# Kernel optimization log

Measured on AMD Instinct MI355X. Metric: run time of the kernel, lower is better.

Reference implementation:

```python
import jax, jax.numpy as jnp
import numpy as np

N = 50000
E = 1600000
D_IN, H1, H2, N_CLS = 512, 128, 64, 10


def _add_self_loops(edge_index, n, edge_attr=None):
    loops = jnp.arange(n, dtype=edge_index.dtype)
    ei = jnp.concatenate([edge_index, jnp.stack([loops, loops])], axis=1)
    if edge_attr is None:
        return ei, None
    # PyG fill_value='mean' for self-loop edge attributes
    loop_attr = jnp.broadcast_to(jnp.mean(edge_attr, axis=0, keepdims=True), (n, edge_attr.shape[1]))
    return ei, jnp.concatenate([edge_attr, loop_attr], axis=0)


def _gat_conv(x, src, dst, n, W, a_src, a_dst, bias, edge_attr=None, We=None, a_edge=None):
    # single-head GATConv
    h = x @ W                                   # (N, out)
    alpha = (h * a_src).sum(-1)[src] + (h * a_dst).sum(-1)[dst]  # (E,)
    if edge_attr is not None:
        alpha = alpha + ((edge_attr @ We) * a_edge).sum(-1)
    alpha = jax.nn.leaky_relu(alpha, 0.2)
    # segment softmax over incoming edges of each dst node
    m = jax.ops.segment_max(alpha, dst, num_segments=n)
    e = jnp.exp(alpha - m[dst])
    s = jax.ops.segment_sum(e, dst, num_segments=n)
    coef = e / (s[dst] + 1e-16)
    out = jax.ops.segment_sum(h[src] * coef[:, None], dst, num_segments=n)
    return out + bias


def _prelu(x, a):
    return jnp.where(x >= 0, x, a * x)


def setup_inputs() -> dict:
    key = jax.random.key(0)
    ks = jax.random.split(key, 24)
    g = lambda k, shape, scale: (jax.random.normal(k, shape, dtype=jnp.float32) * scale)
    inp = {
        "x": jax.random.normal(ks[0], (N, D_IN), dtype=jnp.float32),
        "edge_index": jax.random.randint(ks[1], (2, E), 0, N, dtype=jnp.int32),
        "ppmi_edge_index": jax.random.randint(ks[2], (2, E), 0, N, dtype=jnp.int32),
        "ppmi_edge_attr": jax.random.uniform(ks[3], (E, 1), dtype=jnp.float32),
        # adjacency-branch GAT params
        "W1": g(ks[4], (D_IN, H1), (1.0 / D_IN) ** 0.5),
        "att_src1": g(ks[5], (H1,), 0.1), "att_dst1": g(ks[6], (H1,), 0.1),
        "b1": jnp.zeros((H1,), jnp.float32),
        "W2": g(ks[7], (H1, H2), (1.0 / H1) ** 0.5),
        "att_src2": g(ks[8], (H2,), 0.1), "att_dst2": g(ks[9], (H2,), 0.1),
        "b2": jnp.zeros((H2,), jnp.float32),
        "prelu_a": jnp.float32(0.25),
        # ppmi-branch GAT params (with edge_dim=1)
        "pW1": g(ks[10], (D_IN, H1), (1.0 / D_IN) ** 0.5),
        "patt_src1": g(ks[11], (H1,), 0.1), "patt_dst1": g(ks[12], (H1,), 0.1),
        "pWe1": g(ks[13], (1, H1), 1.0), "patt_e1": g(ks[14], (H1,), 0.1),
        "pb1": jnp.zeros((H1,), jnp.float32),
        "pW2": g(ks[15], (H1, H2), (1.0 / H1) ** 0.5),
        "patt_src2": g(ks[16], (H2,), 0.1), "patt_dst2": g(ks[17], (H2,), 0.1),
        "pWe2": g(ks[18], (1, H2), 1.0), "patt_e2": g(ks[19], (H2,), 0.1),
        "pb2": jnp.zeros((H2,), jnp.float32),
        "pprelu_a": jnp.float32(0.25),
        # fusion attention (Linear(64,1))
        "attn_w": g(ks[20], (H2,), (1.0 / H2) ** 0.5),
        "attn_b": jnp.zeros((), jnp.float32),
        # classifier
        "clf_w": g(ks[21], (H2, N_CLS), (2.0 / H2) ** 0.5),
        "clf_b": jnp.full((N_CLS,), 0.1, jnp.float32),
    }
    return inp


def reference(x, edge_index, ppmi_edge_index, ppmi_edge_attr,
              W1, att_src1, att_dst1, b1, W2, att_src2, att_dst2, b2, prelu_a,
              pW1, patt_src1, patt_dst1, pWe1, patt_e1, pb1,
              pW2, patt_src2, patt_dst2, pWe2, patt_e2, pb2, pprelu_a,
              attn_w, attn_b, clf_w, clf_b):
    n = x.shape[0]
    # adjacency branch (GCN class, GATConv without edge_attr)
    ei, _ = _add_self_loops(edge_index, n)
    src, dst = ei[0], ei[1]
    f1 = _prelu(_gat_conv(x, src, dst, n, W1, att_src1, att_dst1, b1), prelu_a)
    l_out = _prelu(_gat_conv(f1, src, dst, n, W2, att_src2, att_dst2, b2), prelu_a)
    # ppmi branch (GATConv with scalar edge attributes)
    pei, pea = _add_self_loops(ppmi_edge_index, n, ppmi_edge_attr)
    psrc, pdst = pei[0], pei[1]
    g1 = _prelu(_gat_conv(x, psrc, pdst, n, pW1, patt_src1, patt_dst1, pb1, pea, pWe1, patt_e1), pprelu_a)
    g_out = _prelu(_gat_conv(g1, psrc, pdst, n, pW2, patt_src2, patt_dst2, pb2, pea, pWe2, patt_e2), pprelu_a)
    # attn_mode == 1: softmax fusion over stacked branch embeddings
    stacked = jnp.stack([l_out, g_out], axis=1)             # (N, 2, H2)
    scores = stacked @ attn_w + attn_b                      # (N, 2)
    w = jax.nn.softmax(scores, axis=1)[..., None]           # (N, 2, 1)
    emb = jnp.sum(stacked * w, axis=1)                      # (N, H2)
    pred = emb @ clf_w + clf_b                              # (N, n_classes)
    return (emb, pred)
```

## Files before the change

kernel.cpp:

```cpp
#include <hip/hip_runtime.h>
#include <hip/hip_fp16.h>


static constexpr int D_IN = 512;
static constexpr int H1c  = 128;
static constexpr int H2c  = 64;
static constexpr int NCLS = 10;

#define DEV __device__ __forceinline__

DEV float waveReduceSum(float v) {
#pragma unroll
  for (int off = 32; off; off >>= 1) v += __shfl_xor(v, off);
  return v;
}

__global__ void k_sum(const float* __restrict__ x, int n, float* __restrict__ out) {
  float v = 0.f;
  for (int i = blockIdx.x * blockDim.x + threadIdx.x; i < n; i += gridDim.x * blockDim.x)
    v += x[i];
  v = waveReduceSum(v);
  if ((threadIdx.x & 63) == 0) atomicAdd(out, v);
}

__global__ void k_edge_coef(const float* __restrict__ We1, const float* __restrict__ ae1,
                            const float* __restrict__ We2, const float* __restrict__ ae2,
                            float* __restrict__ scal) {
  int lane = threadIdx.x;
  float p1 = We1[lane] * ae1[lane] + We1[lane + 64] * ae1[lane + 64];
  float p2 = We2[lane] * ae2[lane];
  p1 = waveReduceSum(p1);
  p2 = waveReduceSum(p2);
  if (lane == 0) { scal[1] = p1; scal[2] = p2; }
}

__global__ void k_count2(const int* __restrict__ eiA, const int* __restrict__ eiP,
                         int E, int n, int* __restrict__ countsA, int* __restrict__ countsP,
                         int* __restrict__ posA, int* __restrict__ posP) {
  int tot = E + n;
  int tot2 = 2 * tot;
  for (int i = blockIdx.x * blockDim.x + threadIdx.x; i < tot2; i += gridDim.x * blockDim.x) {
    bool isP = i >= tot;
    int e = isP ? i - tot : i;
    const int* ei = isP ? eiP : eiA;
    int* counts = isP ? countsP : countsA;
    int* pos = isP ? posP : posA;
    int d = (e < E) ? ei[(size_t)E + e] : (e - E);
    pos[e] = atomicAdd(&counts[d], 1);
  }
}

__global__ void k_scan_block(const int* __restrict__ counts, int n,
                             int* __restrict__ rowptr, int* __restrict__ blockSums) {
  __shared__ int buf[256];
  int tid = threadIdx.x;
  int i = blockIdx.x * 256 + tid;
  int v = (i < n) ? counts[i] : 0;
  buf[tid] = v;
  __syncthreads();
#pragma unroll
  for (int off = 1; off < 256; off <<= 1) {
    int t = (tid >= off) ? buf[tid - off] : 0;
    __syncthreads();
    buf[tid] += t;
    __syncthreads();
  }
  if (i < n) rowptr[i] = buf[tid] - v;
  if (tid == 255) blockSums[blockIdx.x] = buf[255];
}

__global__ void k_scan_sums(int* __restrict__ bs, int nb) {
  __shared__ int buf[256];
  int tid = threadIdx.x;
  int v = (tid < nb) ? bs[tid] : 0;
  buf[tid] = v;
  __syncthreads();
#pragma unroll
  for (int off = 1; off < 256; off <<= 1) {
    int t = (tid >= off) ? buf[tid - off] : 0;
    __syncthreads();
    buf[tid] += t;
    __syncthreads();
  }
  if (tid < nb) bs[tid] = buf[tid] - v;
  if (tid == 255) bs[nb] = buf[255];
}

__global__ void k_scan_add(int* __restrict__ rowptr, const int* __restrict__ bs, int n, int nb) {
  int i = blockIdx.x * blockDim.x + threadIdx.x;
  if (i < n) rowptr[i] += bs[i >> 8];
  else if (i == n) rowptr[n] = bs[nb];
}

__global__ void k_fill2(const int* __restrict__ eiA, const int* __restrict__ eiP,
                        const float* __restrict__ pea, int E, int n,
                        const int* __restrict__ rowptrA, const int* __restrict__ rowptrP,
                        const int* __restrict__ posA, const int* __restrict__ posP,
                        int* __restrict__ srcsA, int2* __restrict__ packP,
                        const float* __restrict__ scal) {
  int tot = E + n;
  int tot2 = 2 * tot;
  float meanea = scal[0] / (float)E;
  for (int i = blockIdx.x * blockDim.x + threadIdx.x; i < tot2; i += gridDim.x * blockDim.x) {
    if (i < tot) {
      int e = i;
      int s, d;
      if (e < E) { s = eiA[e]; d = eiA[(size_t)E + e]; }
      else { s = d = e - E; }
      int slot = rowptrA[d] + posA[e];
      __builtin_nontemporal_store(s, &srcsA[slot]);
    } else {
      int e = i - tot;
      int s, d;
      float ev;
      if (e < E) { s = eiP[e]; d = eiP[(size_t)E + e]; ev = pea[e]; }
      else { s = d = e - E; ev = meanea; }
      int slot = rowptrP[d] + posP[e];
      unsigned long long u =
          ((unsigned long long)__float_as_uint(ev) << 32) | (unsigned int)s;
      __builtin_nontemporal_store(u, (unsigned long long*)&packP[slot]);
    }
  }
}

template <int BM, int BN, int BK, int TM, int TN>
__global__ __launch_bounds__(256) void gemm_dual_h(const float* __restrict__ A,
                                                   const float* __restrict__ B1,
                                                   const float* __restrict__ B2,
                                                   __half* __restrict__ C1,
                                                   __half* __restrict__ C2,
                                                   int M, int N, int K) {
  __shared__ float As[BK][BM + 4];
  __shared__ float B1s[BK][BN + 4];
  __shared__ float B2s[BK][BN + 4];
  constexpr int TX = BN / TN;
  const int tid = threadIdx.x;
  const int tx = tid % TX;
  const int ty = tid / TX;
  const int rowBase = blockIdx.x * BM;
  const int colBase = blockIdx.y * BN;
  float acc1[TM][TN] = {}, acc2[TM][TN] = {};
  constexpr int A4 = (BM * BK / 4) / 256;
  constexpr int B4 = (BN * BK / 4) / 256;
  for (int k0 = 0; k0 < K; k0 += BK) {
#pragma unroll
    for (int it = 0; it < A4; ++it) {
      int idx = it * 256 + tid;
      int row = idx / (BK / 4);
      int cv = (idx % (BK / 4)) * 4;
      int gr = rowBase + row;
      float4 v = make_float4(0.f, 0.f, 0.f, 0.f);
      if (gr < M) v = *(const float4*)(A + (size_t)gr * K + k0 + cv);
      As[cv + 0][row] = v.x;
      As[cv + 1][row] = v.y;
      As[cv + 2][row] = v.z;
      As[cv + 3][row] = v.w;
    }
#pragma unroll
    for (int it = 0; it < B4; ++it) {
      int idx = it * 256 + tid;
      int r = idx / (BN / 4);
      int c = (idx % (BN / 4)) * 4;
      *(float4*)&B1s[r][c] = *(const float4*)(B1 + (size_t)(k0 + r) * N + colBase + c);
      *(float4*)&B2s[r][c] = *(const float4*)(B2 + (size_t)(k0 + r) * N + colBase + c);
    }
    __syncthreads();
#pragma unroll
    for (int kk = 0; kk < BK; ++kk) {
      float a[TM], b1[TN], b2[TN];
#pragma unroll
      for (int i = 0; i < TM; i += 4) *(float4*)&a[i] = *(const float4*)&As[kk][ty * TM + i];
#pragma unroll
      for (int j = 0; j < TN; j += 4) {
        *(float4*)&b1[j] = *(const float4*)&B1s[kk][tx * TN + j];
        *(float4*)&b2[j] = *(const float4*)&B2s[kk][tx * TN + j];
      }
#pragma unroll
      for (int i = 0; i < TM; ++i)
#pragma unroll
        for (int j = 0; j < TN; ++j) {
          acc1[i][j] = fmaf(a[i], b1[j], acc1[i][j]);
          acc2[i][j] = fmaf(a[i], b2[j], acc2[i][j]);
        }
    }
    __syncthreads();
  }
#pragma unroll
  for (int i = 0; i < TM; ++i) {
    int gr = rowBase + ty * TM + i;
    if (gr < M) {
      __half* c1p = C1 + (size_t)gr * N + colBase + tx * TN;
      __half* c2p = C2 + (size_t)gr * N + colBase + tx * TN;
#pragma unroll
      for (int j = 0; j < TN; j += 2) {
        *(__half2*)&c1p[j] = __floats2half2_rn(acc1[i][j], acc1[i][j + 1]);
        *(__half2*)&c2p[j] = __floats2half2_rn(acc2[i][j], acc2[i][j + 1]);
      }
    }
  }
}

template <int BM, int BN, int BK, int TM, int TN>
__global__ __launch_bounds__(256) void gemm_pair_h(const float* __restrict__ A0,
                                                   const float* __restrict__ A1,
                                                   const float* __restrict__ B0,
                                                   const float* __restrict__ B1,
                                                   __half* __restrict__ C0,
                                                   __half* __restrict__ C1,
                                                   int M, int N, int K) {
  const float* A = blockIdx.z ? A1 : A0;
  const float* B = blockIdx.z ? B1 : B0;
  __half* C = blockIdx.z ? C1 : C0;
  __shared__ float As[BK][BM + 4];
  __shared__ float Bs[BK][BN + 4];
  constexpr int TX = BN / TN;
  const int tid = threadIdx.x;
  const int tx = tid % TX;
  const int ty = tid / TX;
  const int rowBase = blockIdx.x * BM;
  const int colBase = blockIdx.y * BN;
  float acc[TM][TN] = {};
  constexpr int A4 = (BM * BK / 4) / 256;
  constexpr int B4 = (BN * BK / 4) / 256;
  for (int k0 = 0; k0 < K; k0 += BK) {
#pragma unroll
    for (int it = 0; it < A4; ++it) {
      int idx = it * 256 + tid;
      int row = idx / (BK / 4);
      int cv = (idx % (BK / 4)) * 4;
      int gr = rowBase + row;
      float4 v = make_float4(0.f, 0.f, 0.f, 0.f);
      if (gr < M) v = *(const float4*)(A + (size_t)gr * K + k0 + cv);
      As[cv + 0][row] = v.x;
      As[cv + 1][row] = v.y;
      As[cv + 2][row] = v.z;
      As[cv + 3][row] = v.w;
    }
#pragma unroll
    for (int it = 0; it < B4; ++it) {
      int idx = it * 256 + tid;
      int r = idx / (BN / 4);
      int c = (idx % (BN / 4)) * 4;
      *(float4*)&Bs[r][c] = *(const float4*)(B + (size_t)(k0 + r) * N + colBase + c);
    }
    __syncthreads();
#pragma unroll
    for (int kk = 0; kk < BK; ++kk) {
      float a[TM], b[TN];
#pragma unroll
      for (int i = 0; i < TM; i += 4) *(float4*)&a[i] = *(const float4*)&As[kk][ty * TM + i];
#pragma unroll
      for (int j = 0; j < TN; j += 4) *(float4*)&b[j] = *(const float4*)&Bs[kk][tx * TN + j];
#pragma unroll
      for (int i = 0; i < TM; ++i)
#pragma unroll
        for (int j = 0; j < TN; ++j) acc[i][j] = fmaf(a[i], b[j], acc[i][j]);
    }
    __syncthreads();
  }
#pragma unroll
  for (int i = 0; i < TM; ++i) {
    int gr = rowBase + ty * TM + i;
    if (gr < M) {
      __half* cp = C + (size_t)gr * N + colBase + tx * TN;
#pragma unroll
      for (int j = 0; j < TN; j += 2)
        *(__half2*)&cp[j] = __floats2half2_rn(acc[i][j], acc[i][j + 1]);
    }
  }
}

template <int DIM>
__global__ void k_node_dots2(const __half* __restrict__ hA, const __half* __restrict__ hP,
                             const float* __restrict__ vaA, const float* __restrict__ vbA,
                             const float* __restrict__ vaP, const float* __restrict__ vbP,
                             float* __restrict__ asA, float* __restrict__ adA,
                             float* __restrict__ asP, float* __restrict__ adP, int n) {
  int wid = (blockIdx.x * blockDim.x + threadIdx.x) >> 6;
  int lane = threadIdx.x & 63;
  if (wid >= n) return;
  bool isP = blockIdx.y != 0;
  const __half* h = isP ? hP : hA;
  const float* va = isP ? vaP : vaA;
  const float* vb = isP ? vbP : vbA;
  float* oa = isP ? asP : asA;
  float* ob = isP ? adP : adA;
  const __half* hr = h + (size_t)wid * DIM;
  float pa = 0.f, pb = 0.f;
#pragma unroll
  for (int v = 0; v < DIM / 64; ++v) {
    float xv = __half2float(hr[lane + 64 * v]);
    pa += xv * va[lane + 64 * v];
    pb += xv * vb[lane + 64 * v];
  }
  pa = waveReduceSum(pa);
  pb = waveReduceSum(pb);
  if (lane == 0) { oa[wid] = pa; ob[wid] = pb; }
}

DEV float leaky02(float a) { return a > 0.f ? a : 0.2f * a; }
DEV float expw(float a) { return __expf(fminf(a, 80.f)); }

template <int DIM>
__global__ void k_gat_agg2(const __half* __restrict__ hA, const __half* __restrict__ hP,
                           const int* __restrict__ rowptrA, const int* __restrict__ rowptrP,
                           const int* __restrict__ srcsA, const int2* __restrict__ packP,
                           const float* __restrict__ scal, int scal_idx,
                           const float* __restrict__ asA, const float* __restrict__ adA,
                           const float* __restrict__ asP, const float* __restrict__ adP,
                           const float* __restrict__ biasA, const float* __restrict__ biasP,
                           const float* __restrict__ paA, const float* __restrict__ paP,
                           float* __restrict__ outA, float* __restrict__ outP, int n) {
  int wid = (blockIdx.x * blockDim.x + threadIdx.x) >> 6;
  int lane = threadIdx.x & 63;
  if (wid >= n) return;
  bool isP = blockIdx.y != 0;
  const char* hb = (const char*)(isP ? hP : hA);
  const int* rowptr = isP ? rowptrP : rowptrA;
  const float* as_ = isP ? asP : asA;
  const float* bias = isP ? biasP : biasA;
  float* outp = isP ? outP : outA;
  float adv = (isP ? adP : adA)[wid];
  float pa = (isP ? paP : paA)[0];
  float c = isP ? scal[scal_idx] : 0.f;
  int e0 = rowptr[wid], e1 = rowptr[wid + 1];
  float ssum = 0.f;
  float accx = 0.f, accy = 0.f;
  const unsigned lb = (DIM == 128) ? ((unsigned)lane << 2) : ((unsigned)lane << 1);
  for (int base = e0; base < e1; base += 64) {
    int ee = base + lane;
    float w = 0.f;
    int s = 0;
    if (ee < e1) {
      float a;
      if (isP) {
        int2 p = packP[ee];
        s = p.x;
        a = c * __int_as_float(p.y);
      } else {
        s = srcsA[ee];
        a = 0.f;
      }
      a += as_[s] + adv;
      w = expw(leaky02(a));
    }
    ssum += w;
    int cnt = min(64, e1 - base);
    int j = 0;
    for (; j + 4 <= cnt; j += 4) {
      float w0 = __shfl(w, j), w1 = __shfl(w, j + 1);
      float w2 = __shfl(w, j + 2), w3 = __shfl(w, j + 3);
      int s0 = __shfl(s, j), s1 = __shfl(s, j + 1);
      int s2 = __shfl(s, j + 2), s3 = __shfl(s, j + 3);
      if constexpr (DIM == 128) {
        __half2 v0 = *(const __half2*)(hb + (((unsigned)s0 << 8) + lb));
        __half2 v1 = *(const __half2*)(hb + (((unsigned)s1 << 8) + lb));
        __half2 v2 = *(const __half2*)(hb + (((unsigned)s2 << 8) + lb));
        __half2 v3 = *(const __half2*)(hb + (((unsigned)s3 << 8) + lb));
        float2 f0 = __half22float2(v0), f1 = __half22float2(v1);
        float2 f2 = __half22float2(v2), f3 = __half22float2(v3);
        accx += w0 * f0.x + w1 * f1.x + w2 * f2.x + w3 * f3.x;
        accy += w0 * f0.y + w1 * f1.y + w2 * f2.y + w3 * f3.y;
      } else {
        float f0 = __half2float(*(const __half*)(hb + (((unsigned)s0 << 7) + lb)));
        float f1 = __half2float(*(const __half*)(hb + (((unsigned)s1 << 7) + lb)));
        float f2 = __half2float(*(const __half*)(hb + (((unsigned)s2 << 7) + lb)));
        float f3 = __half2float(*(const __half*)(hb + (((unsigned)s3 << 7) + lb)));
        accx += w0 * f0 + w1 * f1 + w2 * f2 + w3 * f3;
      }
    }
    for (; j < cnt; ++j) {
      float wj = __shfl(w, j);
      int sj = __shfl(s, j);
      if constexpr (DIM == 128) {
        float2 f = __half22float2(*(const __half2*)(hb + (((unsigned)sj << 8) + lb)));
        accx += wj * f.x;
        accy += wj * f.y;
      } else {
        accx += wj * __half2float(*(const __half*)(hb + (((unsigned)sj << 7) + lb)));
      }
    }
  }
  ssum = waveReduceSum(ssum);
  float inv = 1.f / (ssum + 1e-16f);
  if constexpr (DIM == 128) {
    float2 bv = ((const float2*)bias)[lane];
    float ox = accx * inv + bv.x;
    float oy = accy * inv + bv.y;
    ox = ox >= 0.f ? ox : pa * ox;
    oy = oy >= 0.f ? oy : pa * oy;
    ((float2*)(outp + (size_t)wid * 128))[lane] = make_float2(ox, oy);
  } else {
    float o = accx * inv + bias[lane];
    o = o >= 0.f ? o : pa * o;
    outp[(size_t)wid * 64 + lane] = o;
  }
}

__global__ void k_fuse(const float* __restrict__ lout, const float* __restrict__ gout,
                       const float* __restrict__ attn_w, const float* __restrict__ attn_b,
                       const float* __restrict__ clf_w, const float* __restrict__ clf_b,
                       float* __restrict__ out, int n) {
  int wid = (blockIdx.x * blockDim.x + threadIdx.x) >> 6;
  int lane = threadIdx.x & 63;
  if (wid >= n) return;
  float l = lout[(size_t)wid * 64 + lane];
  float g = gout[(size_t)wid * 64 + lane];
  float aw = attn_w[lane];
  float s0 = waveReduceSum(l * aw) + attn_b[0];
  float s1 = waveReduceSum(g * aw) + attn_b[0];
  float mx = fmaxf(s0, s1);
  float e0 = __expf(s0 - mx), e1 = __expf(s1 - mx);
  float inv = 1.f / (e0 + e1);
  float w0 = e0 * inv, w1 = e1 * inv;
  float emb = w0 * l + w1 * g;
  out[(size_t)wid * 64 + lane] = emb;
  float p[NCLS];
#pragma unroll
  for (int cc = 0; cc < NCLS; ++cc) p[cc] = emb * clf_w[lane * NCLS + cc];
#pragma unroll
  for (int off = 32; off; off >>= 1)
#pragma unroll
    for (int cc = 0; cc < NCLS; ++cc) p[cc] += __shfl_xor(p[cc], off);
  if (lane < NCLS) {
    float val = 0.f;
#pragma unroll
    for (int cc = 0; cc < NCLS; ++cc)
      if (lane == cc) val = p[cc];
    out[(size_t)n * 64 + (size_t)wid * NCLS + lane] = val + clf_b[lane];
  }
}

extern "C" void kernel_launch(void* const* d_in, const int* in_sizes, int n_in,
                              void* d_out, int out_size, void* d_ws, size_t ws_size,
                              hipStream_t stream) {
  const float* x         = (const float*)d_in[0];
  const int*   ei        = (const int*)d_in[1];
  const int*   pei       = (const int*)d_in[2];
  const float* pea       = (const float*)d_in[3];
  const float* W1        = (const float*)d_in[4];
  const float* att_src1  = (const float*)d_in[5];
  const float* att_dst1  = (const float*)d_in[6];
  const float* b1        = (const float*)d_in[7];
  const float* W2        = (const float*)d_in[8];
  const float* att_src2  = (const float*)d_in[9];
  const float* att_dst2  = (const float*)d_in[10];
  const float* b2        = (const float*)d_in[11];
  const float* prelu_a   = (const float*)d_in[12];
  const float* pW1       = (const float*)d_in[13];
  const float* patt_src1 = (const float*)d_in[14];
  const float* patt_dst1 = (const float*)d_in[15];
  const float* pWe1      = (const float*)d_in[16];
  const float* patt_e1   = (const float*)d_in[17];
  const float* pb1       = (const float*)d_in[18];
  const float* pW2       = (const float*)d_in[19];
  const float* patt_src2 = (const float*)d_in[20];
  const float* patt_dst2 = (const float*)d_in[21];
  const float* pWe2      = (const float*)d_in[22];
  const float* patt_e2   = (const float*)d_in[23];
  const float* pb2       = (const float*)d_in[24];
  const float* pprelu_a  = (const float*)d_in[25];
  const float* attn_w    = (const float*)d_in[26];
  const float* attn_b    = (const float*)d_in[27];
  const float* clf_w     = (const float*)d_in[28];
  const float* clf_b     = (const float*)d_in[29];
  float* out = (float*)d_out;

  const int N = in_sizes[0] / D_IN;
  const int E = in_sizes[1] / 2;
  const int Etot = E + N;

  char* wsp = (char*)d_ws;
  size_t used = 0;
  auto alloc = [&](size_t bytes) {
    char* p = wsp + used;
    used += (bytes + 255) & ~(size_t)255;
    return p;
  };
  __half* h1a_h = (__half*)alloc((size_t)N * H1c * 2);
  __half* h1p_h = (__half*)alloc((size_t)N * H1c * 2);
  float*  f1a   = (float*)alloc((size_t)N * H1c * 4);
  float*  g1p   = (float*)alloc((size_t)N * H1c * 4);
  __half* h2a_h = (__half*)alloc((size_t)N * H2c * 2);
  __half* h2p_h = (__half*)alloc((size_t)N * H2c * 2);
  float*  as_a  = (float*)alloc((size_t)N * 4);
  float*  ad_a  = (float*)alloc((size_t)N * 4);
  float*  as_p  = (float*)alloc((size_t)N * 4);
  float*  ad_p  = (float*)alloc((size_t)N * 4);
  float*  scal  = (float*)alloc(64);
  int*    rowptrA = (int*)alloc((size_t)(N + 1) * 4);
  int*    rowptrP = (int*)alloc((size_t)(N + 1) * 4);
  int*    countsA = (int*)alloc((size_t)N * 4);
  int*    countsP = (int*)alloc((size_t)N * 4);
  int*    blockSums = (int*)alloc(513 * 4);
  int*    srcsA = (int*)alloc((size_t)Etot * 4);
  int2*   packP = (int2*)alloc((size_t)Etot * 8);
  int* posA = (int*)f1a;
  int* posP = posA + Etot;
  float* l_out = (float*)h1a_h;
  float* g_out = (float*)h1p_h;
  if (used > ws_size) return;

  hipMemsetAsync(countsA, 0, sizeof(int) * (size_t)N, stream);
  hipMemsetAsync(countsP, 0, sizeof(int) * (size_t)N, stream);
  hipMemsetAsync(scal, 0, 64, stream);

  const int GS = 2048;
  k_sum<<<1024, 256, 0, stream>>>(pea, E, scal);
  k_edge_coef<<<1, 64, 0, stream>>>(pWe1, patt_e1, pWe2, patt_e2, scal);

  k_count2<<<GS, 256, 0, stream>>>(ei, pei, E, N, countsA, countsP, posA, posP);
  int nb = (N + 255) / 256;
  int scanAddBlocks = (N + 1 + 255) / 256;
  k_scan_block<<<nb, 256, 0, stream>>>(countsA, N, rowptrA, blockSums);
  k_scan_sums<<<1, 256, 0, stream>>>(blockSums, nb);
  k_scan_add<<<scanAddBlocks, 256, 0, stream>>>(rowptrA, blockSums, N, nb);
  k_scan_block<<<nb, 256, 0, stream>>>(countsP, N, rowptrP, blockSums);
  k_scan_sums<<<1, 256, 0, stream>>>(blockSums, nb);
  k_scan_add<<<scanAddBlocks, 256, 0, stream>>>(rowptrP, blockSums, N, nb);
  k_fill2<<<GS, 256, 0, stream>>>(ei, pei, pea, E, N, rowptrA, rowptrP, posA, posP,
                                  srcsA, packP, scal);

  dim3 g1((N + 127) / 128, H1c / 64);
  gemm_dual_h<128, 64, 32, 8, 4><<<g1, 256, 0, stream>>>(x, W1, pW1, h1a_h, h1p_h,
                                                         N, H1c, D_IN);
  int gw = (N + 3) / 4;
  dim3 gd(gw, 2);
  k_node_dots2<H1c><<<gd, 256, 0, stream>>>(h1a_h, h1p_h, att_src1, att_dst1, patt_src1,
                                            patt_dst1, as_a, ad_a, as_p, ad_p, N);
  k_gat_agg2<H1c><<<gd, 256, 0, stream>>>(h1a_h, h1p_h, rowptrA, rowptrP, srcsA, packP,
                                          scal, 1, as_a, ad_a, as_p, ad_p, b1, pb1,
                                          prelu_a, pprelu_a, f1a, g1p, N);

  dim3 g2((N + 63) / 64, H2c / 64, 2);
  gemm_pair_h<64, 64, 32, 4, 4><<<g2, 256, 0, stream>>>(f1a, g1p, W2, pW2, h2a_h, h2p_h,
                                                        N, H2c, H1c);
  k_node_dots2<H2c><<<gd, 256, 0, stream>>>(h2a_h, h2p_h, att_src2, att_dst2, patt_src2,
                                            patt_dst2, as_a, ad_a, as_p, ad_p, N);
  k_gat_agg2<H2c><<<gd, 256, 0, stream>>>(h2a_h, h2p_h, rowptrA, rowptrP, srcsA, packP,
                                          scal, 2, as_a, ad_a, as_p, ad_p, b2, pb2,
                                          prelu_a, pprelu_a, l_out, g_out, N);

  k_fuse<<<gw, 256, 0, stream>>>(l_out, g_out, attn_w, attn_b, clf_w, clf_b, out, N);
}
```

Measured before the change: 1.004 ms.

## Replace scalar FP32 first-layer dual GEMM with fp16 MFMA wave-tiled kernel

Replaces the shared-memory FP32 SIMT dual GEMM (x @ W1 and x @ pW1) with a kernel that uses 16x16x32 fp16 MFMA instructions. Each wave owns 16 rows and converts x to fp16 on the fly. Weights are pre-transposed and converted to fp16 by a small new kernel. This targets the FMA-bound first-layer projection, but reduces input precision to fp16, drops the shared-memory reuse of B, and relies on N being a multiple of 16 because there is no row bounds check.

```diff
diff --git a/kernel.cpp b/kernel.cpp
--- a/kernel.cpp
+++ b/kernel.cpp
@@ -6,6 +6,9 @@
 static constexpr int H1c  = 128;
 static constexpr int H2c  = 64;
 static constexpr int NCLS = 10;
+
+typedef _Float16 f16x8v __attribute__((ext_vector_type(8)));
+typedef float f32x4v __attribute__((ext_vector_type(4)));
 
 #define DEV __device__ __forceinline__
 
@@ -123,79 +126,68 @@
   }
 }
 
-template <int BM, int BN, int BK, int TM, int TN>
-__global__ __launch_bounds__(256) void gemm_dual_h(const float* __restrict__ A,
-                                                   const float* __restrict__ B1,
-                                                   const float* __restrict__ B2,
-                                                   __half* __restrict__ C1,
-                                                   __half* __restrict__ C2,
-                                                   int M, int N, int K) {
-  __shared__ float As[BK][BM + 4];
-  __shared__ float B1s[BK][BN + 4];
-  __shared__ float B2s[BK][BN + 4];
-  constexpr int TX = BN / TN;
-  const int tid = threadIdx.x;
-  const int tx = tid % TX;
-  const int ty = tid / TX;
-  const int rowBase = blockIdx.x * BM;
-  const int colBase = blockIdx.y * BN;
-  float acc1[TM][TN] = {}, acc2[TM][TN] = {};
-  constexpr int A4 = (BM * BK / 4) / 256;
-  constexpr int B4 = (BN * BK / 4) / 256;
-  for (int k0 = 0; k0 < K; k0 += BK) {
-#pragma unroll
-    for (int it = 0; it < A4; ++it) {
-      int idx = it * 256 + tid;
-      int row = idx / (BK / 4);
-      int cv = (idx % (BK / 4)) * 4;
-      int gr = rowBase + row;
-      float4 v = make_float4(0.f, 0.f, 0.f, 0.f);
-      if (gr < M) v = *(const float4*)(A + (size_t)gr * K + k0 + cv);
-      As[cv + 0][row] = v.x;
-      As[cv + 1][row] = v.y;
-      As[cv + 2][row] = v.z;
-      As[cv + 3][row] = v.w;
-    }
-#pragma unroll
-    for (int it = 0; it < B4; ++it) {
-      int idx = it * 256 + tid;
-      int r = idx / (BN / 4);
-      int c = (idx % (BN / 4)) * 4;
-      *(float4*)&B1s[r][c] = *(const float4*)(B1 + (size_t)(k0 + r) * N + colBase + c);
-      *(float4*)&B2s[r][c] = *(const float4*)(B2 + (size_t)(k0 + r) * N + colBase + c);
-    }
-    __syncthreads();
-#pragma unroll
-    for (int kk = 0; kk < BK; ++kk) {
-      float a[TM], b1[TN], b2[TN];
-#pragma unroll
-      for (int i = 0; i < TM; i += 4) *(float4*)&a[i] = *(const float4*)&As[kk][ty * TM + i];
-#pragma unroll
-      for (int j = 0; j < TN; j += 4) {
-        *(float4*)&b1[j] = *(const float4*)&B1s[kk][tx * TN + j];
-        *(float4*)&b2[j] = *(const float4*)&B2s[kk][tx * TN + j];
-      }
-#pragma unroll
-      for (int i = 0; i < TM; ++i)
-#pragma unroll
-        for (int j = 0; j < TN; ++j) {
-          acc1[i][j] = fmaf(a[i], b1[j], acc1[i][j]);
-          acc2[i][j] = fmaf(a[i], b2[j], acc2[i][j]);
-        }
-    }
-    __syncthreads();
-  }
-#pragma unroll
-  for (int i = 0; i < TM; ++i) {
-    int gr = rowBase + ty * TM + i;
-    if (gr < M) {
-      __half* c1p = C1 + (size_t)gr * N + colBase + tx * TN;
-      __half* c2p = C2 + (size_t)gr * N + colBase + tx * TN;
-#pragma unroll
-      for (int j = 0; j < TN; j += 2) {
-        *(__half2*)&c1p[j] = __floats2half2_rn(acc1[i][j], acc1[i][j + 1]);
-        *(__half2*)&c2p[j] = __floats2half2_rn(acc2[i][j], acc2[i][j + 1]);
-      }
+__global__ void k_wconv(const float* __restrict__ W1, const float* __restrict__ W2,
+                        _Float16* __restrict__ Wt1, _Float16* __restrict__ Wt2,
+                        int K, int N) {
+  int tot = K * N;
+  for (int i = blockIdx.x * blockDim.x + threadIdx.x; i < 2 * tot;
+       i += gridDim.x * blockDim.x) {
+    bool second = i >= tot;
+    int e = second ? i - tot : i;
+    int k = e / N, n = e % N;
+    float v = (second ? W2 : W1)[e];
+    (second ? Wt2 : Wt1)[n * K + k] = (_Float16)v;
+  }
+}
+
+template <int NCOLS>
+__global__ __launch_bounds__(256) void mfma_dual(const float* __restrict__ A,
+                                                 const _Float16* __restrict__ Wt1,
+                                                 const _Float16* __restrict__ Wt2,
+                                                 __half* __restrict__ C1,
+                                                 __half* __restrict__ C2,
+                                                 int M, int K) {
+  constexpr int NB = NCOLS / 16;
+  int wid = (int)((blockIdx.x * blockDim.x + threadIdx.x) >> 6);
+  int lane = threadIdx.x & 63;
+  int rowTile = wid * 16;
+  if (rowTile >= M) return;
+  int l15 = lane & 15;
+  int kb = lane >> 4;
+  const float* ap = A + (size_t)(rowTile + l15) * K + kb * 8;
+  const _Float16* b1p = Wt1 + (size_t)l15 * K + kb * 8;
+  const _Float16* b2p = Wt2 + (size_t)l15 * K + kb * 8;
+  f32x4v acc1[NB], acc2[NB];
+#pragma unroll
+  for (int nb = 0; nb < NB; ++nb) {
+    f32x4v z = {0.f, 0.f, 0.f, 0.f};
+    acc1[nb] = z;
+    acc2[nb] = z;
+  }
+  for (int k0 = 0; k0 < K; k0 += 32) {
+    float4 a0 = *(const float4*)(ap + k0);
+    float4 a1 = *(const float4*)(ap + k0 + 4);
+    f16x8v af;
+    af[0] = (_Float16)a0.x; af[1] = (_Float16)a0.y;
+    af[2] = (_Float16)a0.z; af[3] = (_Float16)a0.w;
+    af[4] = (_Float16)a1.x; af[5] = (_Float16)a1.y;
+    af[6] = (_Float16)a1.z; af[7] = (_Float16)a1.w;
+#pragma unroll
+    for (int nb = 0; nb < NB; ++nb) {
+      f16x8v b1 = *(const f16x8v*)(b1p + (size_t)nb * 16 * K + k0);
+      f16x8v b2 = *(const f16x8v*)(b2p + (size_t)nb * 16 * K + k0);
+      acc1[nb] = __builtin_amdgcn_mfma_f32_16x16x32_f16(af, b1, acc1[nb], 0, 0, 0);
+      acc2[nb] = __builtin_amdgcn_mfma_f32_16x16x32_f16(af, b2, acc2[nb], 0, 0, 0);
+    }
+  }
+  int orow = rowTile + kb * 4;
+#pragma unroll
+  for (int nb = 0; nb < NB; ++nb) {
+    int oc = nb * 16 + l15;
+#pragma unroll
+    for (int j = 0; j < 4; ++j) {
+      C1[(size_t)(orow + j) * NCOLS + oc] = __float2half(acc1[nb][j]);
+      C2[(size_t)(orow + j) * NCOLS + oc] = __float2half(acc2[nb][j]);
     }
   }
 }
@@ -495,6 +487,8 @@
   int*    blockSums = (int*)alloc(513 * 4);
   int*    srcsA = (int*)alloc((size_t)Etot * 4);
   int2*   packP = (int2*)alloc((size_t)Etot * 8);
+  _Float16* Wt1 = (_Float16*)alloc((size_t)D_IN * H1c * 2);
+  _Float16* Wt2 = (_Float16*)alloc((size_t)D_IN * H1c * 2);
   int* posA = (int*)f1a;
   int* posP = posA + Etot;
   float* l_out = (float*)h1a_h;
@@ -508,6 +502,7 @@
   const int GS = 2048;
   k_sum<<<1024, 256, 0, stream>>>(pea, E, scal);
   k_edge_coef<<<1, 64, 0, stream>>>(pWe1, patt_e1, pWe2, patt_e2, scal);
+  k_wconv<<<64, 256, 0, stream>>>(W1, pW1, Wt1, Wt2, D_IN, H1c);
 
   k_count2<<<GS, 256, 0, stream>>>(ei, pei, E, N, countsA, countsP, posA, posP);
   int nb = (N + 255) / 256;
@@ -521,9 +516,9 @@
   k_fill2<<<GS, 256, 0, stream>>>(ei, pei, pea, E, N, rowptrA, rowptrP, posA, posP,
                                   srcsA, packP, scal);
 
-  dim3 g1((N + 127) / 128, H1c / 64);
-  gemm_dual_h<128, 64, 32, 8, 4><<<g1, 256, 0, stream>>>(x, W1, pW1, h1a_h, h1p_h,
-                                                         N, H1c, D_IN);
+  int nwaves = (N + 15) / 16;
+  int mblocks = (nwaves * 64 + 255) / 256;
+  mfma_dual<H1c><<<mblocks, 256, 0, stream>>>(x, Wt1, Wt2, h1a_h, h1p_h, N, D_IN);
   int gw = (N + 3) / 4;
   dim3 gd(gw, 2);
   k_node_dots2<H1c><<<gd, 256, 0, stream>>>(h1a_h, h1p_h, att_src1, att_dst1, patt_src1,
```

Result: faster. 953.0 us (-5.0%).
